# Kernel optimization log

Measured on AMD Instinct MI355X. Metric: run time of the kernel, lower is better.

Reference implementation:

```python
import jax, jax.numpy as jnp
import numpy as np

B, T = 8192, 26
V, E, H, L = 23, 100, 128, 64  # vocab, emb dim, GRU hidden, latent; LSTM hidden = E


def setup_inputs() -> dict:
    key = jax.random.key(0)
    ks = jax.random.split(key, 16)
    rn = lambda k, shape, scale=0.1: (jax.random.normal(k, shape, jnp.float32) * scale)
    emb = rn(ks[0], (V, E)).at[0].set(0.0)  # padding_idx=0 row zeroed
    return {
        "z": jax.random.normal(ks[1], (B, L), jnp.float32),
        "x_in": jax.random.randint(ks[2], (B, T), 0, V),
        "emb": emb,
        "fc_z_w": rn(ks[3], (H, L)), "fc_z_b": rn(ks[4], (H,)),
        "gru_wih": rn(ks[5], (3 * H, E)), "gru_whh": rn(ks[6], (3 * H, H)),
        "gru_bih": rn(ks[7], (3 * H,)), "gru_bhh": rn(ks[8], (3 * H,)),
        "lstm_wih": rn(ks[9], (4 * E, H)), "lstm_whh": rn(ks[10], (4 * E, E)),
        "lstm_bih": rn(ks[11], (4 * E,)), "lstm_bhh": rn(ks[12], (4 * E,)),
        "out_w": rn(ks[13], (V, E)), "out_b": rn(ks[14], (V,)),
    }


def _gru(e, h0, Wih, Whh, bih, bhh):
    # e: (B,T,E); precompute input projections for all steps, scan over T.
    xg = jnp.einsum('bti,gi->btg', e, Wih) + bih  # (B,T,3H)

    def step(h, x):
        hg = h @ Whh.T + bhh
        xr, xz, xn = jnp.split(x, 3, axis=-1)
        hr, hz, hn = jnp.split(hg, 3, axis=-1)
        r = jax.nn.sigmoid(xr + hr)
        zg = jax.nn.sigmoid(xz + hz)
        n = jnp.tanh(xn + r * hn)
        h_new = (1.0 - zg) * n + zg * h
        return h_new, h_new

    _, ys = jax.lax.scan(step, h0, jnp.swapaxes(xg, 0, 1))  # (T,B,H)
    return jnp.swapaxes(ys, 0, 1)


def _lstm(x, h0, c0, Wih, Whh, bih, bhh):
    xg = jnp.einsum('bti,gi->btg', x, Wih) + bih  # (B,T,4E)

    def step(hc, xt):
        h, c = hc
        g = xt + h @ Whh.T + bhh
        i, f, gg, o = jnp.split(g, 4, axis=-1)
        c_new = jax.nn.sigmoid(f) * c + jax.nn.sigmoid(i) * jnp.tanh(gg)
        h_new = jax.nn.sigmoid(o) * jnp.tanh(c_new)
        return (h_new, c_new), h_new

    _, ys = jax.lax.scan(step, (h0, c0), jnp.swapaxes(xg, 0, 1))
    return jnp.swapaxes(ys, 0, 1)


def reference(z, x_in, emb, fc_z_w, fc_z_b, gru_wih, gru_whh, gru_bih, gru_bhh,
              lstm_wih, lstm_whh, lstm_bih, lstm_bhh, out_w, out_b):
    h0 = jnp.tanh(z @ fc_z_w.T + fc_z_b)            # (B,H)
    e = emb[x_in]                                    # (B,T,E)
    y = _gru(e, h0, gru_wih, gru_whh, gru_bih, gru_bhh)           # (B,T,H)
    zeros = jnp.zeros((z.shape[0], E), dtype=z.dtype)
    y = _lstm(y, zeros, zeros, lstm_wih, lstm_whh, lstm_bih, lstm_bhh)  # (B,T,E)
    logits = jnp.einsum('bte,ve->btv', y, out_w) + out_b          # (B,T,V)
    return logits
```

## Files before the change

### kernel.cpp

```cpp
#include <hip/hip_runtime.h>
#include <stdint.h>
#include <stddef.h>

#define BB 8192
#define TT 26
#define VV 23
#define EE 100
#define HH 128
#define LL 64

typedef __attribute__((ext_vector_type(8))) short bf16x8;
typedef __attribute__((ext_vector_type(4))) float f32x4;

#define MFMA(a, b, c) __builtin_amdgcn_mfma_f32_16x16x32_bf16((a), (b), (c), 0, 0, 0)

#define OFF_GRUW   0ull
#define OFF_TBL    98304ull
#define OFF_LSTMW  122880ull
#define OFF_OUTW   352256ull
#define OFF_FCZW   360448ull
#define OFF_LBIAS  376832ull
#define OFF_Y      379904ull

__device__ __forceinline__ void force_frag(bf16x8& v) { asm volatile("" : "+v"(v)); }

__device__ __forceinline__ unsigned short f2bf(float f) {
  union { float f; unsigned u; } v; v.f = f;
  unsigned u = v.u;
  return (unsigned short)((u + 0x7FFFu + ((u >> 16) & 1u)) >> 16);
}
__device__ __forceinline__ unsigned short f2bf_fast(float f) {
  union { float f; unsigned u; } v; v.f = f;
  return (unsigned short)((v.u + 0x8000u) >> 16);
}
#define LOG2E 1.4426950408889634f
__device__ __forceinline__ float sigm(float x) {
  return __builtin_amdgcn_rcpf(1.0f + __builtin_amdgcn_exp2f(-x * LOG2E));
}
__device__ __forceinline__ float tanh_(float x) {
  return __builtin_fmaf(-2.0f,
      __builtin_amdgcn_rcpf(1.0f + __builtin_amdgcn_exp2f(x * (2.0f * LOG2E))), 1.0f);
}

__global__ __launch_bounds__(256) void prep_kernel(
    const float* __restrict__ emb, const float* __restrict__ fc_z_w,
    const float* __restrict__ gru_wih, const float* __restrict__ gru_whh,
    const float* __restrict__ gru_bih,
    const float* __restrict__ lstm_wih, const float* __restrict__ lstm_whh,
    const float* __restrict__ lstm_bih, const float* __restrict__ lstm_bhh,
    const float* __restrict__ out_w,
    char* __restrict__ ws)
{
  int e = blockIdx.x * 256 + threadIdx.x;

  if (e < 49152) {
    int j = e & 7, lane = (e >> 3) & 63, kc = (e >> 9) & 3, ct = e >> 11;
    int n = ct * 16 + (lane & 15);
    int k = kc * 32 + ((lane >> 4) & 3) * 8 + j;
    *(unsigned short*)(ws + OFF_GRUW + (size_t)e * 2) = f2bf(gru_whh[n * HH + k]);
    return;
  }
  e -= 49152;
  if (e < 12288) {
    int j = e & 7, lane = (e >> 3) & 63, ct = e >> 9;
    int n = ct * 16 + (lane & 15);
    int k = ((lane >> 4) & 3) * 8 + j;
    float v = 0.0f;
    if (k < VV) {
      float s0 = 0.f, s1 = 0.f, s2 = 0.f, s3 = 0.f;
      const float* ep = emb + k * EE;
      const float* wp = gru_wih + n * EE;
#pragma unroll 5
      for (int m = 0; m < EE; m += 4) {
        s0 += ep[m] * wp[m];     s1 += ep[m + 1] * wp[m + 1];
        s2 += ep[m + 2] * wp[m + 2]; s3 += ep[m + 3] * wp[m + 3];
      }
      v = gru_bih[n] + ((s0 + s1) + (s2 + s3));
    }
    *(unsigned short*)(ws + OFF_TBL + (size_t)e * 2) = f2bf(v);
    return;
  }
  e -= 12288;
  if (e < 114688) {
    int j = e & 7, lane = (e >> 3) & 63, kc = (e >> 9) & 7, ct = e >> 12;
    int row = ct * 16 + (lane & 15);
    int g = row / 112, c = row % 112;
    int q = (lane >> 4) & 3;
    float v = 0.0f;
    if (c < EE) {
      if (kc < 4) {
        int k = kc * 32 + q * 8 + j;
        v = lstm_wih[(g * EE + c) * HH + k];
      } else {
        int k = (kc - 4) * 32 + q * 8 + j;
        if (k < EE) v = lstm_whh[(g * EE + c) * EE + k];
      }
    }
    *(unsigned short*)(ws + OFF_LSTMW + (size_t)e * 2) = f2bf(v);
    return;
  }
  e -= 114688;
  if (e < 4096) {
    int j = e & 7, lane = (e >> 3) & 63, kc = (e >> 9) & 3, ct = e >> 11;
    int n = ct * 16 + (lane & 15);
    int k = kc * 32 + ((lane >> 4) & 3) * 8 + j;
    float v = (n < VV && k < EE) ? out_w[n * EE + k] : 0.0f;
    *(unsigned short*)(ws + OFF_OUTW + (size_t)e * 2) = f2bf(v);
    return;
  }
  e -= 4096;
  if (e < 8192) {
    int j = e & 7, lane = (e >> 3) & 63, kc = (e >> 9) & 1, ct = e >> 10;
    int n = ct * 16 + (lane & 15);
    int k = kc * 32 + ((lane >> 4) & 3) * 8 + j;
    *(unsigned short*)(ws + OFF_FCZW + (size_t)e * 2) = f2bf(fc_z_w[n * LL + k]);
    return;
  }
  e -= 8192;
  if (e < 448) {
    int g = e / 112, c = e % 112;
    float v = (c < EE) ? (lstm_bih[g * EE + c] + lstm_bhh[g * EE + c]) : 0.0f;
    *(float*)(ws + OFF_LBIAS + (size_t)e * 4) = v;
  }
}

__global__ __launch_bounds__(512, 4) void gru_kernel(
    const float* __restrict__ z, const int* __restrict__ x_in,
    const float* __restrict__ fc_z_b, const float* __restrict__ gru_bhh,
    const unsigned short* __restrict__ gruw, const unsigned short* __restrict__ tbl,
    const unsigned short* __restrict__ fczw, unsigned short* __restrict__ yout)
{
  __shared__ unsigned short hfrag[2][2048];
  __shared__ unsigned char idx_lds[TT * 16];
  const int tid  = threadIdx.x;
  const int wv   = tid >> 6;
  const int lane = tid & 63;
  const int l15  = lane & 15;
  const int q    = (lane >> 4) & 3;
  const int blk  = blockIdx.x;

  for (int i = tid; i < TT * 16; i += 512) {
    int t = i >> 4, r = i & 15;
    idx_lds[i] = (unsigned char)x_in[(blk * 16 + r) * TT + t];
  }

  bf16x8 gw[3][4], tw[3];
#pragma unroll
  for (int g = 0; g < 3; g++) {
    int ct = g * 8 + wv;
#pragma unroll
    for (int kc = 0; kc < 4; kc++) {
      gw[g][kc] = *(const bf16x8*)(gruw + (size_t)(ct * 4 + kc) * 512 + lane * 8);
      force_frag(gw[g][kc]);
    }
    tw[g] = *(const bf16x8*)(tbl + (size_t)ct * 512 + lane * 8);
    force_frag(tw[g]);
  }
  const int col = wv * 16 + l15;
  const float b_r = gru_bhh[0 * HH + col];
  const float b_z = gru_bhh[1 * HH + col];
  const float b_n = gru_bhh[2 * HH + col];
  const int wbase = (col >> 5) * 512 + ((col >> 3) & 3) * 128 + (col & 7);

  float h[4];
  {
    bf16x8 fw0 = *(const bf16x8*)(fczw + (size_t)(wv * 2 + 0) * 512 + lane * 8);
    bf16x8 fw1 = *(const bf16x8*)(fczw + (size_t)(wv * 2 + 1) * 512 + lane * 8);
    const float* zp = z + (size_t)(blk * 16 + l15) * LL + q * 8;
    f32x4 z0 = *(const f32x4*)(zp);
    f32x4 z1 = *(const f32x4*)(zp + 4);
    f32x4 z2 = *(const f32x4*)(zp + 32);
    f32x4 z3 = *(const f32x4*)(zp + 36);
    bf16x8 za0, za1;
#pragma unroll
    for (int j = 0; j < 4; j++) {
      za0[j]     = (short)f2bf(z0[j]);
      za0[4 + j] = (short)f2bf(z1[j]);
      za1[j]     = (short)f2bf(z2[j]);
      za1[4 + j] = (short)f2bf(z3[j]);
    }
    float fzb = fc_z_b[col];
    f32x4 acc = {fzb, fzb, fzb, fzb};
    acc = MFMA(za0, fw0, acc);
    acc = MFMA(za1, fw1, acc);
#pragma unroll
    for (int i = 0; i < 4; i++) {
      h[i] = tanh_(acc[i]);
      hfrag[0][wbase + (q * 4 + i) * 8] = f2bf_fast(h[i]);
    }
  }
  __syncthreads();

  int cur = 0;
  for (int t = 0; t < TT; t++) {
    if (t > 0 && wv < 4) {
      bf16x8 yv = *(const bf16x8*)((const char*)hfrag[cur] + wv * 1024 + lane * 16);
      *(bf16x8*)(yout + ((size_t)(blk * TT + (t - 1)) * 4 + wv) * 512 + lane * 8) = yv;
    }
    int iv = idx_lds[t * 16 + l15];
    bf16x8 oh;
#pragma unroll
    for (int j = 0; j < 8; j++)
      oh[j] = (short)((iv == q * 8 + j) ? 0x3F80 : 0);

    f32x4 ar  = {b_r, b_r, b_r, b_r};
    f32x4 az  = {b_z, b_z, b_z, b_z};
    f32x4 ahn = {b_n, b_n, b_n, b_n};
    f32x4 axn = {0.0f, 0.0f, 0.0f, 0.0f};
    ar  = MFMA(oh, tw[0], ar);
    az  = MFMA(oh, tw[1], az);
    axn = MFMA(oh, tw[2], axn);

    bf16x8 a[4];
#pragma unroll
    for (int kc = 0; kc < 4; kc++)
      a[kc] = *(const bf16x8*)((const char*)hfrag[cur] + kc * 1024 + lane * 16);
#pragma unroll
    for (int kc = 0; kc < 4; kc++) {
      ar  = MFMA(a[kc], gw[0][kc], ar);
      az  = MFMA(a[kc], gw[1][kc], az);
      ahn = MFMA(a[kc], gw[2][kc], ahn);
    }

    int nb = cur ^ 1;
#pragma unroll
    for (int i = 0; i < 4; i++) {
      float r  = sigm(ar[i]);
      float zg = sigm(az[i]);
      float n  = tanh_(__builtin_fmaf(r, ahn[i], axn[i]));
      h[i] = __builtin_fmaf(zg, h[i] - n, n);
      hfrag[nb][wbase + (q * 4 + i) * 8] = f2bf_fast(h[i]);
    }
    __syncthreads();
    cur = nb;
  }
  if (wv < 4) {
    bf16x8 yv = *(const bf16x8*)((const char*)hfrag[cur] + wv * 1024 + lane * 16);
    *(bf16x8*)(yout + ((size_t)(blk * TT + (TT - 1)) * 4 + wv) * 512 + lane * 8) = yv;
  }
}

__global__ __launch_bounds__(896, 4) void lstm_kernel(
    const unsigned short* __restrict__ lstmw, const float* __restrict__ lbias,
    unsigned short* __restrict__ ybuf)
{
  __shared__ float Pbuf[2][4 * 7 * 64 * 4];
  __shared__ unsigned short hbuf[2][2048];
  const int tid  = threadIdx.x;
  const int wv   = tid >> 6;
  const int lane = tid & 63;
  const int l15  = lane & 15;
  const int q    = (lane >> 4) & 3;
  const int blk  = blockIdx.x;

  for (int i = tid; i < 4096; i += 896)
    ((unsigned short*)hbuf)[i] = 0;
  __syncthreads();

  if (wv < 7) {
    bf16x8 lwy[4][4];
#pragma unroll
    for (int g = 0; g < 4; g++)
#pragma unroll
      for (int kc = 0; kc < 4; kc++) {
        lwy[g][kc] = *(const bf16x8*)(lstmw + (size_t)((g * 7 + wv) * 8 + kc) * 512 + lane * 8);
        force_frag(lwy[g][kc]);
      }
    const int col = wv * 16 + l15;
    float b[4];
#pragma unroll
    for (int g = 0; g < 4; g++) b[g] = lbias[g * 112 + col];

    bf16x8 ya[4];
#pragma unroll
    for (int kc = 0; kc < 4; kc++)
      ya[kc] = *(const bf16x8*)(ybuf + ((size_t)(blk * TT + 0) * 4 + kc) * 512 + lane * 8);

    for (int p = 0; p < TT + 2; p++) {
      if (p >= 2 && wv < 4) {
        bf16x8 hv = *(const bf16x8*)((const char*)hbuf[p & 1] + wv * 1024 + lane * 16);
        *(bf16x8*)(ybuf + ((size_t)(blk * TT + (p - 2)) * 4 + wv) * 512 + lane * 8) = hv;
      }
      if (p <= TT - 1) {
#pragma unroll
        for (int g = 0; g < 4; g++) {
          f32x4 acc = {b[g], b[g], b[g], b[g]};
#pragma unroll
          for (int kc = 0; kc < 4; kc++)
            acc = MFMA(ya[kc], lwy[g][kc], acc);
          *(f32x4*)&Pbuf[p & 1][((g * 7 + wv) * 64 + lane) * 4] = acc;
        }
        if (p < TT - 1) {
#pragma unroll
          for (int kc = 0; kc < 4; kc++)
            ya[kc] = *(const bf16x8*)(ybuf + ((size_t)(blk * TT + p + 1) * 4 + kc) * 512 + lane * 8);
        }
      }
      __syncthreads();
    }
  } else {
    const int tile = wv - 7;
    bf16x8 lwh[4][4];
#pragma unroll
    for (int g = 0; g < 4; g++)
#pragma unroll
      for (int kc = 0; kc < 4; kc++) {
        lwh[g][kc] = *(const bf16x8*)(lstmw + (size_t)((g * 7 + tile) * 8 + kc + 4) * 512 + lane * 8);
        force_frag(lwh[g][kc]);
      }
    const int col = tile * 16 + l15;
    const int wbase = (col >> 5) * 512 + ((col >> 3) & 3) * 128 + (col & 7);
    float c[4] = {0, 0, 0, 0};

    for (int p = 0; p < TT + 2; p++) {
      if (p >= 1 && p <= TT) {
        const int rb = (p - 1) & 1;
        f32x4 ai = *(const f32x4*)&Pbuf[rb][((0 * 7 + tile) * 64 + lane) * 4];
        f32x4 af = *(const f32x4*)&Pbuf[rb][((1 * 7 + tile) * 64 + lane) * 4];
        f32x4 ag = *(const f32x4*)&Pbuf[rb][((2 * 7 + tile) * 64 + lane) * 4];
        f32x4 ao = *(const f32x4*)&Pbuf[rb][((3 * 7 + tile) * 64 + lane) * 4];
        bf16x8 ha[4];
#pragma unroll
        for (int kc = 0; kc < 4; kc++)
          ha[kc] = *(const bf16x8*)((const char*)hbuf[p & 1] + kc * 1024 + lane * 16);
#pragma unroll
        for (int kc = 0; kc < 4; kc++) {
          ai = MFMA(ha[kc], lwh[0][kc], ai);
          af = MFMA(ha[kc], lwh[1][kc], af);
          ag = MFMA(ha[kc], lwh[2][kc], ag);
          ao = MFMA(ha[kc], lwh[3][kc], ao);
        }
#pragma unroll
        for (int i = 0; i < 4; i++) {
          float ii = sigm(ai[i]), ff = sigm(af[i]);
          float gg = tanh_(ag[i]), oo = sigm(ao[i]);
          float cn = __builtin_fmaf(ff, c[i], ii * gg);
          c[i] = cn;
          hbuf[rb][wbase + (q * 4 + i) * 8] = f2bf_fast(oo * tanh_(cn));
        }
      }
      __syncthreads();
    }
  }
}

__global__ __launch_bounds__(512) void logits_kernel(
    const float* __restrict__ out_b, const unsigned short* __restrict__ hg,
    const unsigned short* __restrict__ outw, float* __restrict__ out)
{
  const int tid  = threadIdx.x;
  const int wv   = tid >> 6;
  const int lane = tid & 63;
  const int l15  = lane & 15;
  const int q    = (lane >> 4) & 3;
  const int blk  = blockIdx.x;

  bf16x8 ow[2][4];
#pragma unroll
  for (int ct = 0; ct < 2; ct++)
#pragma unroll
    for (int kc = 0; kc < 4; kc++) {
      ow[ct][kc] = *(const bf16x8*)(outw + (size_t)(ct * 4 + kc) * 512 + lane * 8);
      force_frag(ow[ct][kc]);
    }
  float ob[2];
#pragma unroll
  for (int ct = 0; ct < 2; ct++) {
    int cv = ct * 16 + l15;
    ob[ct] = (cv < VV) ? out_b[cv] : 0.0f;
  }

  for (int t = wv; t < TT; t += 8) {
    bf16x8 ha[4];
#pragma unroll
    for (int kc = 0; kc < 4; kc++)
      ha[kc] = *(const bf16x8*)(hg + ((size_t)(blk * TT + t) * 4 + kc) * 512 + lane * 8);
#pragma unroll
    for (int ct = 0; ct < 2; ct++) {
      f32x4 acc = {ob[ct], ob[ct], ob[ct], ob[ct]};
#pragma unroll
      for (int kc = 0; kc < 4; kc++)
        acc = MFMA(ha[kc], ow[ct][kc], acc);
      int cv = ct * 16 + l15;
      if (cv < VV) {
#pragma unroll
        for (int i = 0; i < 4; i++) {
          int rowg = blk * 16 + q * 4 + i;
          out[((size_t)rowg * TT + t) * VV + cv] = acc[i];
        }
      }
    }
  }
}

extern "C" void kernel_launch(void* const* d_in, const int* in_sizes, int n_in,
                              void* d_out, int out_size, void* d_ws, size_t ws_size,
                              hipStream_t stream) {
  (void)in_sizes; (void)n_in; (void)out_size; (void)ws_size;
  const float* z        = (const float*)d_in[0];
  const int*   x_in     = (const int*)  d_in[1];
  const float* emb      = (const float*)d_in[2];
  const float* fc_z_w   = (const float*)d_in[3];
  const float* fc_z_b   = (const float*)d_in[4];
  const float* gru_wih  = (const float*)d_in[5];
  const float* gru_whh  = (const float*)d_in[6];
  const float* gru_bih  = (const float*)d_in[7];
  const float* gru_bhh  = (const float*)d_in[8];
  const float* lstm_wih = (const float*)d_in[9];
  const float* lstm_whh = (const float*)d_in[10];
  const float* lstm_bih = (const float*)d_in[11];
  const float* lstm_bhh = (const float*)d_in[12];
  const float* out_w    = (const float*)d_in[13];
  const float* out_b    = (const float*)d_in[14];
  char*  ws  = (char*)d_ws;
  float* out = (float*)d_out;

  const unsigned short* gruw  = (const unsigned short*)(ws + OFF_GRUW);
  const unsigned short* tblp  = (const unsigned short*)(ws + OFF_TBL);
  const unsigned short* lstmw = (const unsigned short*)(ws + OFF_LSTMW);
  const unsigned short* outw  = (const unsigned short*)(ws + OFF_OUTW);
  const unsigned short* fczw  = (const unsigned short*)(ws + OFF_FCZW);
  const float*          lbias = (const float*)(ws + OFF_LBIAS);
  unsigned short*       ybuf  = (unsigned short*)(ws + OFF_Y);

  prep_kernel<<<738, 256, 0, stream>>>(emb, fc_z_w, gru_wih, gru_whh, gru_bih,
                                       lstm_wih, lstm_whh, lstm_bih, lstm_bhh,
                                       out_w, ws);
  gru_kernel<<<512, 512, 0, stream>>>(z, x_in, fc_z_b, gru_bhh,
                                      gruw, tblp, fczw, ybuf);
  lstm_kernel<<<512, 896, 0, stream>>>(lstmw, lbias, ybuf);
  logits_kernel<<<512, 512, 0, stream>>>(out_b, ybuf, outw, out);
}
```

Baseline: 209.2 us.

## Process two batch tiles per block, fuse logits into LSTM kernel

The GRU and LSTM kernels now each handle 32 batch rows per block (two 16-row sub-tiles) with 256 blocks, so each wave reuses its register-resident weight fragments across twice the rows. The LSTM kernel drops its producer/consumer wave split: each of 7 waves computes both the input and recurrent projections, and the eighth wave computes logits directly from the LDS hidden state. This removes the separate logits kernel and the round trip of LSTM outputs through global memory. The trade-offs are that each wave's sequential step does twice the work, grid parallelism is halved, and the LSTM waves hold more weight registers.

```diff
diff --git a/kernel.cpp b/kernel.cpp
--- a/kernel.cpp
+++ b/kernel.cpp
@@ -124,14 +124,14 @@
   }
 }
 
-__global__ __launch_bounds__(512, 4) void gru_kernel(
+__global__ __launch_bounds__(512, 2) void gru_kernel(
     const float* __restrict__ z, const int* __restrict__ x_in,
     const float* __restrict__ fc_z_b, const float* __restrict__ gru_bhh,
     const unsigned short* __restrict__ gruw, const unsigned short* __restrict__ tbl,
     const unsigned short* __restrict__ fczw, unsigned short* __restrict__ yout)
 {
-  __shared__ unsigned short hfrag[2][2048];
-  __shared__ unsigned char idx_lds[TT * 16];
+  __shared__ unsigned short hfrag[2][2][2048];
+  __shared__ unsigned char idx_lds[TT * 32];
   const int tid  = threadIdx.x;
   const int wv   = tid >> 6;
   const int lane = tid & 63;
@@ -139,9 +139,9 @@
   const int q    = (lane >> 4) & 3;
   const int blk  = blockIdx.x;
 
-  for (int i = tid; i < TT * 16; i += 512) {
-    int t = i >> 4, r = i & 15;
-    idx_lds[i] = (unsigned char)x_in[(blk * 16 + r) * TT + t];
+  for (int i = tid; i < TT * 32; i += 512) {
+    int t = i >> 5, r = i & 31;
+    idx_lds[i] = (unsigned char)x_in[(blk * 32 + r) * TT + t];
   }
 
   bf16x8 gw[3][4], tw[3];
@@ -162,90 +162,97 @@
   const float b_n = gru_bhh[2 * HH + col];
   const int wbase = (col >> 5) * 512 + ((col >> 3) & 3) * 128 + (col & 7);
 
-  float h[4];
+  float h[2][4];
   {
     bf16x8 fw0 = *(const bf16x8*)(fczw + (size_t)(wv * 2 + 0) * 512 + lane * 8);
     bf16x8 fw1 = *(const bf16x8*)(fczw + (size_t)(wv * 2 + 1) * 512 + lane * 8);
-    const float* zp = z + (size_t)(blk * 16 + l15) * LL + q * 8;
-    f32x4 z0 = *(const f32x4*)(zp);
-    f32x4 z1 = *(const f32x4*)(zp + 4);
-    f32x4 z2 = *(const f32x4*)(zp + 32);
-    f32x4 z3 = *(const f32x4*)(zp + 36);
-    bf16x8 za0, za1;
-#pragma unroll
-    for (int j = 0; j < 4; j++) {
-      za0[j]     = (short)f2bf(z0[j]);
-      za0[4 + j] = (short)f2bf(z1[j]);
-      za1[j]     = (short)f2bf(z2[j]);
-      za1[4 + j] = (short)f2bf(z3[j]);
-    }
     float fzb = fc_z_b[col];
-    f32x4 acc = {fzb, fzb, fzb, fzb};
-    acc = MFMA(za0, fw0, acc);
-    acc = MFMA(za1, fw1, acc);
-#pragma unroll
-    for (int i = 0; i < 4; i++) {
-      h[i] = tanh_(acc[i]);
-      hfrag[0][wbase + (q * 4 + i) * 8] = f2bf_fast(h[i]);
+#pragma unroll
+    for (int s = 0; s < 2; s++) {
+      const float* zp = z + (size_t)(blk * 32 + s * 16 + l15) * LL + q * 8;
+      f32x4 z0 = *(const f32x4*)(zp);
+      f32x4 z1 = *(const f32x4*)(zp + 4);
+      f32x4 z2 = *(const f32x4*)(zp + 32);
+      f32x4 z3 = *(const f32x4*)(zp + 36);
+      bf16x8 za0, za1;
+#pragma unroll
+      for (int j = 0; j < 4; j++) {
+        za0[j]     = (short)f2bf(z0[j]);
+        za0[4 + j] = (short)f2bf(z1[j]);
+        za1[j]     = (short)f2bf(z2[j]);
+        za1[4 + j] = (short)f2bf(z3[j]);
+      }
+      f32x4 acc = {fzb, fzb, fzb, fzb};
+      acc = MFMA(za0, fw0, acc);
+      acc = MFMA(za1, fw1, acc);
+#pragma unroll
+      for (int i = 0; i < 4; i++) {
+        h[s][i] = tanh_(acc[i]);
+        hfrag[0][s][wbase + (q * 4 + i) * 8] = f2bf_fast(h[s][i]);
+      }
     }
   }
   __syncthreads();
 
+  const int xs = wv >> 2, xk = wv & 3;
   int cur = 0;
   for (int t = 0; t < TT; t++) {
-    if (t > 0 && wv < 4) {
-      bf16x8 yv = *(const bf16x8*)((const char*)hfrag[cur] + wv * 1024 + lane * 16);
-      *(bf16x8*)(yout + ((size_t)(blk * TT + (t - 1)) * 4 + wv) * 512 + lane * 8) = yv;
-    }
-    int iv = idx_lds[t * 16 + l15];
-    bf16x8 oh;
-#pragma unroll
-    for (int j = 0; j < 8; j++)
-      oh[j] = (short)((iv == q * 8 + j) ? 0x3F80 : 0);
-
-    f32x4 ar  = {b_r, b_r, b_r, b_r};
-    f32x4 az  = {b_z, b_z, b_z, b_z};
-    f32x4 ahn = {b_n, b_n, b_n, b_n};
-    f32x4 axn = {0.0f, 0.0f, 0.0f, 0.0f};
-    ar  = MFMA(oh, tw[0], ar);
-    az  = MFMA(oh, tw[1], az);
-    axn = MFMA(oh, tw[2], axn);
-
-    bf16x8 a[4];
-#pragma unroll
-    for (int kc = 0; kc < 4; kc++)
-      a[kc] = *(const bf16x8*)((const char*)hfrag[cur] + kc * 1024 + lane * 16);
-#pragma unroll
-    for (int kc = 0; kc < 4; kc++) {
-      ar  = MFMA(a[kc], gw[0][kc], ar);
-      az  = MFMA(a[kc], gw[1][kc], az);
-      ahn = MFMA(a[kc], gw[2][kc], ahn);
-    }
-
+    if (t > 0) {
+      bf16x8 yv = *(const bf16x8*)&hfrag[cur][xs][xk * 512 + lane * 8];
+      *(bf16x8*)(yout + ((size_t)((blk * 2 + xs) * TT + (t - 1)) * 4 + xk) * 512 + lane * 8) = yv;
+    }
     int nb = cur ^ 1;
 #pragma unroll
-    for (int i = 0; i < 4; i++) {
-      float r  = sigm(ar[i]);
-      float zg = sigm(az[i]);
-      float n  = tanh_(__builtin_fmaf(r, ahn[i], axn[i]));
-      h[i] = __builtin_fmaf(zg, h[i] - n, n);
-      hfrag[nb][wbase + (q * 4 + i) * 8] = f2bf_fast(h[i]);
+    for (int s = 0; s < 2; s++) {
+      int iv = idx_lds[t * 32 + s * 16 + l15];
+      bf16x8 oh;
+#pragma unroll
+      for (int j = 0; j < 8; j++)
+        oh[j] = (short)((iv == q * 8 + j) ? 0x3F80 : 0);
+
+      f32x4 ar  = {b_r, b_r, b_r, b_r};
+      f32x4 az  = {b_z, b_z, b_z, b_z};
+      f32x4 ahn = {b_n, b_n, b_n, b_n};
+      f32x4 axn = {0.0f, 0.0f, 0.0f, 0.0f};
+      ar  = MFMA(oh, tw[0], ar);
+      az  = MFMA(oh, tw[1], az);
+      axn = MFMA(oh, tw[2], axn);
+
+      bf16x8 a[4];
+#pragma unroll
+      for (int kc = 0; kc < 4; kc++)
+        a[kc] = *(const bf16x8*)&hfrag[cur][s][kc * 512 + lane * 8];
+#pragma unroll
+      for (int kc = 0; kc < 4; kc++) {
+        ar  = MFMA(a[kc], gw[0][kc], ar);
+        az  = MFMA(a[kc], gw[1][kc], az);
+        ahn = MFMA(a[kc], gw[2][kc], ahn);
+      }
+#pragma unroll
+      for (int i = 0; i < 4; i++) {
+        float r  = sigm(ar[i]);
+        float zg = sigm(az[i]);
+        float n  = tanh_(__builtin_fmaf(r, ahn[i], axn[i]));
+        h[s][i] = __builtin_fmaf(zg, h[s][i] - n, n);
+        hfrag[nb][s][wbase + (q * 4 + i) * 8] = f2bf_fast(h[s][i]);
+      }
     }
     __syncthreads();
     cur = nb;
   }
-  if (wv < 4) {
-    bf16x8 yv = *(const bf16x8*)((const char*)hfrag[cur] + wv * 1024 + lane * 16);
-    *(bf16x8*)(yout + ((size_t)(blk * TT + (TT - 1)) * 4 + wv) * 512 + lane * 8) = yv;
-  }
-}
-
-__global__ __launch_bounds__(896, 4) void lstm_kernel(
+  {
+    bf16x8 yv = *(const bf16x8*)&hfrag[cur][xs][xk * 512 + lane * 8];
+    *(bf16x8*)(yout + ((size_t)((blk * 2 + xs) * TT + (TT - 1)) * 4 + xk) * 512 + lane * 8) = yv;
+  }
+}
+
+__global__ __launch_bounds__(512, 2) void lstm_kernel(
     const unsigned short* __restrict__ lstmw, const float* __restrict__ lbias,
-    unsigned short* __restrict__ ybuf)
+    const unsigned short* __restrict__ ybuf,
+    const float* __restrict__ out_b, const unsigned short* __restrict__ outw,
+    float* __restrict__ out)
 {
-  __shared__ float Pbuf[2][4 * 7 * 64 * 4];
-  __shared__ unsigned short hbuf[2][2048];
+  __shared__ unsigned short hbuf[2][2][2048];
   const int tid  = threadIdx.x;
   const int wv   = tid >> 6;
   const int lane = tid & 63;
@@ -253,142 +260,115 @@
   const int q    = (lane >> 4) & 3;
   const int blk  = blockIdx.x;
 
-  for (int i = tid; i < 4096; i += 896)
+  for (int i = tid; i < 2 * 2 * 2048; i += 512)
     ((unsigned short*)hbuf)[i] = 0;
-  __syncthreads();
 
   if (wv < 7) {
-    bf16x8 lwy[4][4];
+    bf16x8 lw[4][8];
 #pragma unroll
     for (int g = 0; g < 4; g++)
 #pragma unroll
-      for (int kc = 0; kc < 4; kc++) {
-        lwy[g][kc] = *(const bf16x8*)(lstmw + (size_t)((g * 7 + wv) * 8 + kc) * 512 + lane * 8);
-        force_frag(lwy[g][kc]);
+      for (int kc = 0; kc < 8; kc++) {
+        lw[g][kc] = *(const bf16x8*)(lstmw + (size_t)((g * 7 + wv) * 8 + kc) * 512 + lane * 8);
+        force_frag(lw[g][kc]);
       }
     const int col = wv * 16 + l15;
     float b[4];
 #pragma unroll
     for (int g = 0; g < 4; g++) b[g] = lbias[g * 112 + col];
-
-    bf16x8 ya[4];
-#pragma unroll
-    for (int kc = 0; kc < 4; kc++)
-      ya[kc] = *(const bf16x8*)(ybuf + ((size_t)(blk * TT + 0) * 4 + kc) * 512 + lane * 8);
-
-    for (int p = 0; p < TT + 2; p++) {
-      if (p >= 2 && wv < 4) {
-        bf16x8 hv = *(const bf16x8*)((const char*)hbuf[p & 1] + wv * 1024 + lane * 16);
-        *(bf16x8*)(ybuf + ((size_t)(blk * TT + (p - 2)) * 4 + wv) * 512 + lane * 8) = hv;
-      }
-      if (p <= TT - 1) {
-#pragma unroll
-        for (int g = 0; g < 4; g++) {
-          f32x4 acc = {b[g], b[g], b[g], b[g]};
+    const int wbase = (col >> 5) * 512 + ((col >> 3) & 3) * 128 + (col & 7);
+    float c[2][4] = {{0, 0, 0, 0}, {0, 0, 0, 0}};
+    __syncthreads();
+
+    for (int p = 0; p <= TT; p++) {
+      if (p < TT) {
+        bf16x8 ya[2][4];
+#pragma unroll
+        for (int s = 0; s < 2; s++)
 #pragma unroll
           for (int kc = 0; kc < 4; kc++)
-            acc = MFMA(ya[kc], lwy[g][kc], acc);
-          *(f32x4*)&Pbuf[p & 1][((g * 7 + wv) * 64 + lane) * 4] = acc;
+            ya[s][kc] = *(const bf16x8*)(ybuf + ((size_t)((blk * 2 + s) * TT + p) * 4 + kc) * 512 + lane * 8);
+
+#pragma unroll
+        for (int s = 0; s < 2; s++) {
+          bf16x8 ha[4];
+#pragma unroll
+          for (int kc = 0; kc < 4; kc++)
+            ha[kc] = *(const bf16x8*)&hbuf[p & 1][s][kc * 512 + lane * 8];
+          f32x4 ai = {b[0], b[0], b[0], b[0]};
+          f32x4 af = {b[1], b[1], b[1], b[1]};
+          f32x4 ag = {b[2], b[2], b[2], b[2]};
+          f32x4 ao = {b[3], b[3], b[3], b[3]};
+#pragma unroll
+          for (int kc = 0; kc < 4; kc++) {
+            ai = MFMA(ha[kc], lw[0][kc + 4], ai);
+            af = MFMA(ha[kc], lw[1][kc + 4], af);
+            ag = MFMA(ha[kc], lw[2][kc + 4], ag);
+            ao = MFMA(ha[kc], lw[3][kc + 4], ao);
+          }
+#pragma unroll
+          for (int kc = 0; kc < 4; kc++) {
+            ai = MFMA(ya[s][kc], lw[0][kc], ai);
+            af = MFMA(ya[s][kc], lw[1][kc], af);
+            ag = MFMA(ya[s][kc], lw[2][kc], ag);
+            ao = MFMA(ya[s][kc], lw[3][kc], ao);
+          }
+#pragma unroll
+          for (int i = 0; i < 4; i++) {
+            float ii = sigm(ai[i]), ff = sigm(af[i]);
+            float gg = tanh_(ag[i]), oo = sigm(ao[i]);
+            float cn = __builtin_fmaf(ff, c[s][i], ii * gg);
+            c[s][i] = cn;
+            hbuf[(p + 1) & 1][s][wbase + (q * 4 + i) * 8] = f2bf_fast(oo * tanh_(cn));
+          }
         }
-        if (p < TT - 1) {
+      }
+      __syncthreads();
+    }
+  } else {
+    bf16x8 ow[2][4];
+#pragma unroll
+    for (int ct = 0; ct < 2; ct++)
+#pragma unroll
+      for (int kc = 0; kc < 4; kc++) {
+        ow[ct][kc] = *(const bf16x8*)(outw + (size_t)(ct * 4 + kc) * 512 + lane * 8);
+        force_frag(ow[ct][kc]);
+      }
+    float ob[2];
+#pragma unroll
+    for (int ct = 0; ct < 2; ct++) {
+      int cv = ct * 16 + l15;
+      ob[ct] = (cv < VV) ? out_b[cv] : 0.0f;
+    }
+    __syncthreads();
+
+    for (int p = 0; p <= TT; p++) {
+      if (p >= 1) {
+        const int t = p - 1;
+#pragma unroll
+        for (int s = 0; s < 2; s++) {
+          bf16x8 ha[4];
 #pragma unroll
           for (int kc = 0; kc < 4; kc++)
-            ya[kc] = *(const bf16x8*)(ybuf + ((size_t)(blk * TT + p + 1) * 4 + kc) * 512 + lane * 8);
+            ha[kc] = *(const bf16x8*)&hbuf[p & 1][s][kc * 512 + lane * 8];
+#pragma unroll
+          for (int ct = 0; ct < 2; ct++) {
+            f32x4 acc = {ob[ct], ob[ct], ob[ct], ob[ct]};
+#pragma unroll
+            for (int kc = 0; kc < 4; kc++)
+              acc = MFMA(ha[kc], ow[ct][kc], acc);
+            int cv = ct * 16 + l15;
+            if (cv < VV) {
+#pragma unroll
+              for (int i = 0; i < 4; i++) {
+                int rowg = blk * 32 + s * 16 + q * 4 + i;
+                out[((size_t)rowg * TT + t) * VV + cv] = acc[i];
+              }
+            }
+          }
         }
       }
       __syncthreads();
-    }
-  } else {
-    const int tile = wv - 7;
-    bf16x8 lwh[4][4];
-#pragma unroll
-    for (int g = 0; g < 4; g++)
-#pragma unroll
-      for (int kc = 0; kc < 4; kc++) {
-        lwh[g][kc] = *(const bf16x8*)(lstmw + (size_t)((g * 7 + tile) * 8 + kc + 4) * 512 + lane * 8);
-        force_frag(lwh[g][kc]);
-      }
-    const int col = tile * 16 + l15;
-    const int wbase = (col >> 5) * 512 + ((col >> 3) & 3) * 128 + (col & 7);
-    float c[4] = {0, 0, 0, 0};
-
-    for (int p = 0; p < TT + 2; p++) {
-      if (p >= 1 && p <= TT) {
-        const int rb = (p - 1) & 1;
-        f32x4 ai = *(const f32x4*)&Pbuf[rb][((0 * 7 + tile) * 64 + lane) * 4];
-        f32x4 af = *(const f32x4*)&Pbuf[rb][((1 * 7 + tile) * 64 + lane) * 4];
-        f32x4 ag = *(const f32x4*)&Pbuf[rb][((2 * 7 + tile) * 64 + lane) * 4];
-        f32x4 ao = *(const f32x4*)&Pbuf[rb][((3 * 7 + tile) * 64 + lane) * 4];
-        bf16x8 ha[4];
-#pragma unroll
-        for (int kc = 0; kc < 4; kc++)
-          ha[kc] = *(const bf16x8*)((const char*)hbuf[p & 1] + kc * 1024 + lane * 16);
-#pragma unroll
-        for (int kc = 0; kc < 4; kc++) {
-          ai = MFMA(ha[kc], lwh[0][kc], ai);
-          af = MFMA(ha[kc], lwh[1][kc], af);
-          ag = MFMA(ha[kc], lwh[2][kc], ag);
-          ao = MFMA(ha[kc], lwh[3][kc], ao);
-        }
-#pragma unroll
-        for (int i = 0; i < 4; i++) {
-          float ii = sigm(ai[i]), ff = sigm(af[i]);
-          float gg = tanh_(ag[i]), oo = sigm(ao[i]);
-          float cn = __builtin_fmaf(ff, c[i], ii * gg);
-          c[i] = cn;
-          hbuf[rb][wbase + (q * 4 + i) * 8] = f2bf_fast(oo * tanh_(cn));
-        }
-      }
-      __syncthreads();
-    }
-  }
-}
-
-__global__ __launch_bounds__(512) void logits_kernel(
-    const float* __restrict__ out_b, const unsigned short* __restrict__ hg,
-    const unsigned short* __restrict__ outw, float* __restrict__ out)
-{
-  const int tid  = threadIdx.x;
-  const int wv   = tid >> 6;
-  const int lane = tid & 63;
-  const int l15  = lane & 15;
-  const int q    = (lane >> 4) & 3;
-  const int blk  = blockIdx.x;
-
-  bf16x8 ow[2][4];
-#pragma unroll
-  for (int ct = 0; ct < 2; ct++)
-#pragma unroll
-    for (int kc = 0; kc < 4; kc++) {
-      ow[ct][kc] = *(const bf16x8*)(outw + (size_t)(ct * 4 + kc) * 512 + lane * 8);
-      force_frag(ow[ct][kc]);
-    }
-  float ob[2];
-#pragma unroll
-  for (int ct = 0; ct < 2; ct++) {
-    int cv = ct * 16 + l15;
-    ob[ct] = (cv < VV) ? out_b[cv] : 0.0f;
-  }
-
-  for (int t = wv; t < TT; t += 8) {
-    bf16x8 ha[4];
-#pragma unroll
-    for (int kc = 0; kc < 4; kc++)
-      ha[kc] = *(const bf16x8*)(hg + ((size_t)(blk * TT + t) * 4 + kc) * 512 + lane * 8);
-#pragma unroll
-    for (int ct = 0; ct < 2; ct++) {
-      f32x4 acc = {ob[ct], ob[ct], ob[ct], ob[ct]};
-#pragma unroll
-      for (int kc = 0; kc < 4; kc++)
-        acc = MFMA(ha[kc], ow[ct][kc], acc);
-      int cv = ct * 16 + l15;
-      if (cv < VV) {
-#pragma unroll
-        for (int i = 0; i < 4; i++) {
-          int rowg = blk * 16 + q * 4 + i;
-          out[((size_t)rowg * TT + t) * VV + cv] = acc[i];
-        }
-      }
     }
   }
 }
@@ -426,8 +406,7 @@
   prep_kernel<<<738, 256, 0, stream>>>(emb, fc_z_w, gru_wih, gru_whh, gru_bih,
                                        lstm_wih, lstm_whh, lstm_bih, lstm_bhh,
                                        out_w, ws);
-  gru_kernel<<<512, 512, 0, stream>>>(z, x_in, fc_z_b, gru_bhh,
+  gru_kernel<<<256, 512, 0, stream>>>(z, x_in, fc_z_b, gru_bhh,
                                       gruw, tblp, fczw, ybuf);
-  lstm_kernel<<<512, 896, 0, stream>>>(lstmw, lbias, ybuf);
-  logits_kernel<<<512, 512, 0, stream>>>(out_b, ybuf, outw, out);
-}
+  lstm_kernel<<<256, 512, 0, stream>>>(lstmw, lbias, ybuf, out_b, outw, out);
+}
```

New measurement: 207.9 us. Within noise of the previous version (-0.6%).
